# Kernel tuning notes

Measured on AMD Instinct MI355X. Metric: run time of the kernel, lower is better.

Reference implementation:

```python
import jax, jax.numpy as jnp
import numpy as np

IN_F, OUT_F, GROUP = 4096, 4096, 128
N_GROUPS = IN_F // GROUP  # 32


def setup_inputs() -> dict:
    key = jax.random.key(0)
    k1, k2, k3, k4, k5 = jax.random.split(key, 5)
    x = jax.random.normal(k1, (2, 1024, IN_F), dtype=jnp.float32)
    w_q = jax.random.randint(k2, (OUT_F, N_GROUPS, GROUP), -128, 128, dtype=jnp.int32)  # int8-range quantized weights
    s_w = jax.random.uniform(k3, (N_GROUPS, OUT_F), dtype=jnp.float32) * 0.01  # per-group, per-out-channel scales
    perm = jax.random.permutation(k4, IN_F).astype(jnp.int64)  # GPTQ activation-order permutation
    bias = jax.random.normal(k5, (OUT_F,), dtype=jnp.float32)
    return {"x": x, "w_q": w_q, "s_w": s_w, "perm": perm, "bias": bias}


def reference(x, w_q, s_w, perm, bias):
    prefix = x.shape[:-1]
    orig_dtype = x.dtype
    xf = x.reshape(-1, IN_F)          # (n, in)
    xf = xf[:, perm]                  # apply GPTQ permutation
    xf = xf.reshape(-1, N_GROUPS, GROUP).astype(jnp.float32)  # (n, g, k)
    wf = w_q.astype(jnp.float32)      # (o, g, k) dequant-to-fp32 weights (pre-scale)
    y_g = jnp.einsum('ngk,ogk->ngo', xf, wf)   # per-group partial products (n, g, o)
    y = jnp.sum(y_g * s_w[None, :, :], axis=1) # apply group scales, reduce groups -> (n, o)
    y = y + bias.astype(y.dtype)
    return y.reshape(*prefix, OUT_F).astype(orig_dtype)
```

## Files before the change

### kernel.cpp

```cpp
#include <hip/hip_runtime.h>
#include <hip/hip_bf16.h>
#include <stdint.h>

#define IN_F   4096
#define OUT_F  4096
#define M_ROWS 2048
#define NG     32
#define GRP    128

typedef __bf16 bf16x8 __attribute__((ext_vector_type(8)));
typedef float  f32x4  __attribute__((ext_vector_type(4)));

typedef const void __attribute__((address_space(1))) cv_g;
typedef void       __attribute__((address_space(3))) v_l;

__device__ __forceinline__ void async16(const void* g, void* l) {
  __builtin_amdgcn_global_load_lds((cv_g*)g, (v_l*)l, 16, 0, 0);
}

__device__ int g_perm_is64;

__global__ void decode_flag(const void* __restrict__ perm_raw) {
  if (threadIdx.x == 0 && blockIdx.x == 0) {
    const int* w = (const int*)perm_raw;
    int ok = 1;
    for (int j = 0; j < 32; ++j) {
      int lo = w[2 * j], hi = w[2 * j + 1];
      if (hi != 0 || lo < 0 || lo >= IN_F) { ok = 0; break; }
    }
    g_perm_is64 = ok;
  }
}

__global__ __launch_bounds__(256) void prep(const float* __restrict__ x,
                                            const int* __restrict__ w_q,
                                            const float* __restrict__ s_w,
                                            const void* __restrict__ perm_raw,
                                            __hip_bfloat16* __restrict__ xp,
                                            __hip_bfloat16* __restrict__ wf) {
  __shared__ float sx[IN_F];
  __shared__ int sflag;
  const int b = blockIdx.x;
  const int t = threadIdx.x;

  if (b < M_ROWS) {
    const int m = b;
    const float* xr = x + (size_t)m * IN_F;
#pragma unroll
    for (int u = 0; u < 4; ++u) {
      int idx = (u * 256 + t) * 4;
      *(float4*)&sx[idx] = *(const float4*)&xr[idx];
    }
    if (t < 64) {
      const int* w = (const int*)perm_raw;
      int j = t & 31;
      int lo = w[2 * j], hi = w[2 * j + 1];
      int cond = (hi == 0 && lo >= 0 && lo < IN_F);
      unsigned long long bal = __ballot(cond);
      if (t == 0) sflag = (bal == ~0ull) ? 1 : 0;
    }
    __syncthreads();
    const int f = sflag;
    const long long* p64 = (const long long*)perm_raw;
    const int*       p32 = (const int*)perm_raw;
    const int jb = t * 16;
    __hip_bfloat16 tmp[16] __attribute__((aligned(16)));
#pragma unroll
    for (int u = 0; u < 16; ++u) {
      int pj = f ? (int)p64[jb + u] : p32[jb + u];
      tmp[u] = __float2bfloat16(sx[pj]);
    }
    *(uint4*)(xp + (size_t)m * IN_F + jb)     = *(const uint4*)&tmp[0];
    *(uint4*)(xp + (size_t)m * IN_F + jb + 8) = *(const uint4*)&tmp[8];
  } else {
    int tt = (b - M_ROWS) * 256 + t;
    int o  = tt >> 9;
    int kb = (tt & 511) << 3;
    float s = s_w[(size_t)(kb >> 7) * OUT_F + o];
    const int* wr = w_q + (size_t)o * IN_F + kb;
    int4 w0 = *(const int4*)wr;
    int4 w1 = *(const int4*)(wr + 4);
    __hip_bfloat16 tmp[8] __attribute__((aligned(16)));
    tmp[0] = __float2bfloat16((float)w0.x * s);
    tmp[1] = __float2bfloat16((float)w0.y * s);
    tmp[2] = __float2bfloat16((float)w0.z * s);
    tmp[3] = __float2bfloat16((float)w0.w * s);
    tmp[4] = __float2bfloat16((float)w1.x * s);
    tmp[5] = __float2bfloat16((float)w1.y * s);
    tmp[6] = __float2bfloat16((float)w1.z * s);
    tmp[7] = __float2bfloat16((float)w1.w * s);
    *(uint4*)(wf + (size_t)o * IN_F + kb) = *(const uint4*)tmp;
  }
}

__global__ __launch_bounds__(256) void gemm_bt(
    const __hip_bfloat16* __restrict__ A,
    const __hip_bfloat16* __restrict__ B,
    const float* __restrict__ bias,
    float* __restrict__ C) {
  __shared__ __hip_bfloat16 sA[128 * 64];
  __shared__ __hip_bfloat16 sB[128 * 64];

  const int tid  = threadIdx.x;
  const int wave = tid >> 6;
  const int lane = tid & 63;
  const int bm = blockIdx.y << 7;
  const int bn = blockIdx.x << 7;
  const int wm = (wave >> 1) << 6;
  const int wn = (wave & 1) << 6;
  const int lrow = lane & 15;
  const int quad = lane >> 4;

  f32x4 acc[4][4] = {};

  const __hip_bfloat16* gA[4];
  const __hip_bfloat16* gB[4];
  __hip_bfloat16* lA[4];
  __hip_bfloat16* lB[4];
#pragma unroll
  for (int h = 0; h < 4; ++h) {
    int L   = h * 256 + wave * 64 + lane;
    int row = L >> 3;
    int kc  = (L & 7) ^ (row & 7);
    gA[h] = A + (size_t)(bm + row) * IN_F + kc * 8;
    gB[h] = B + (size_t)(bn + row) * IN_F + kc * 8;
    lA[h] = &sA[(h * 256 + wave * 64) * 8];
    lB[h] = &sB[(h * 256 + wave * 64) * 8];
  }

  for (int k0 = 0; k0 < IN_F; k0 += 64) {
#pragma unroll
    for (int h = 0; h < 4; ++h) {
      async16(gA[h] + k0, lA[h]);
      async16(gB[h] + k0, lB[h]);
    }
    __syncthreads();

#pragma unroll
    for (int s = 0; s < 2; ++s) {
      const int kcp = ((s << 2) + quad) ^ (lrow & 7);
      bf16x8 af[4], bfr[4];
#pragma unroll
      for (int i = 0; i < 4; ++i)
        af[i] = *(const bf16x8*)&sA[(wm + i * 16 + lrow) * 64 + kcp * 8];
#pragma unroll
      for (int j = 0; j < 4; ++j)
        bfr[j] = *(const bf16x8*)&sB[(wn + j * 16 + lrow) * 64 + kcp * 8];
#pragma unroll
      for (int i = 0; i < 4; ++i)
#pragma unroll
        for (int j = 0; j < 4; ++j)
          acc[i][j] = __builtin_amdgcn_mfma_f32_16x16x32_bf16(af[i], bfr[j], acc[i][j], 0, 0, 0);
    }

    __syncthreads();
  }

#pragma unroll
  for (int i = 0; i < 4; ++i) {
    int row = bm + wm + i * 16 + quad * 4;
#pragma unroll
    for (int j = 0; j < 4; ++j) {
      int col = bn + wn + j * 16 + lrow;
      float bv = bias[col];
#pragma unroll
      for (int r = 0; r < 4; ++r)
        C[(size_t)(row + r) * OUT_F + col] = acc[i][j][r] + bv;
    }
  }
}

__global__ void naive_fallback(const float* __restrict__ x, const int* __restrict__ w_q,
                               const float* __restrict__ s_w, const void* __restrict__ perm_raw,
                               const float* __restrict__ bias, float* __restrict__ out) {
  int t = blockIdx.x * blockDim.x + threadIdx.x;
  int m = t >> 12;
  int o = t & 4095;
  const int f = g_perm_is64;
  const long long* p64 = (const long long*)perm_raw;
  const int*       p32 = (const int*)perm_raw;
  const float* xr = x + (size_t)m * IN_F;
  const int*   wr = w_q + (size_t)o * IN_F;
  float acc = 0.f;
  for (int g = 0; g < NG; ++g) {
    float part = 0.f;
    for (int k = 0; k < GRP; ++k) {
      int j = g * GRP + k;
      int pj = f ? (int)p64[j] : p32[j];
      part += xr[pj] * (float)wr[j];
    }
    acc += part * s_w[(size_t)g * OUT_F + o];
  }
  out[t] = acc + bias[o];
}

extern "C" void kernel_launch(void* const* d_in, const int* in_sizes, int n_in,
                              void* d_out, int out_size, void* d_ws, size_t ws_size,
                              hipStream_t stream) {
  const float* x    = (const float*)d_in[0];
  const int*   w_q  = (const int*)d_in[1];
  const float* s_w  = (const float*)d_in[2];
  const void*  perm = d_in[3];
  const float* bias = (const float*)d_in[4];
  float* out = (float*)d_out;

  const size_t xp_bytes = (size_t)M_ROWS * IN_F * sizeof(__hip_bfloat16);
  const size_t wf_bytes = (size_t)OUT_F * IN_F * sizeof(__hip_bfloat16);

  if (ws_size < xp_bytes + wf_bytes) {
    decode_flag<<<1, 64, 0, stream>>>(perm);
    naive_fallback<<<(M_ROWS * OUT_F) / 256, 256, 0, stream>>>(x, w_q, s_w, perm, bias, out);
    return;
  }

  __hip_bfloat16* xp = (__hip_bfloat16*)d_ws;
  __hip_bfloat16* wf = (__hip_bfloat16*)((char*)d_ws + xp_bytes);

  prep<<<M_ROWS + (OUT_F * IN_F / 8) / 256, 256, 0, stream>>>(x, w_q, s_w, perm, xp, wf);

  dim3 grid(OUT_F / 128, M_ROWS / 128);
  gemm_bt<<<grid, 256, 0, stream>>>(xp, wf, bias, out);
}
```

Before: 219.7 us.

## Switch GEMM to int8 MFMA with per-row activation quantization and group-scale epilogue

The prep kernel now quantizes each permuted activation row to int8 using a per-row absmax scale, and narrows the int32 weights to raw int8 instead of dequantizing them to bf16. The GEMM runs int8 16x16x64 MFMAs into an int32 accumulator for each 128-wide group, then folds in that group's bf16-stored weight scale and the row scale in fp32. Loads are double-buffered in LDS with 256-wide K stages. The aim is to double MFMA throughput and halve operand traffic, at the cost of extra accuracy loss from int8 activations and per-group epilogue FMAs.

Result: faster. 195.4 us (-11.1%).

```diff
diff --git a/kernel.cpp b/kernel.cpp
--- a/kernel.cpp
+++ b/kernel.cpp
@@ -8,8 +8,8 @@
 #define NG     32
 #define GRP    128
 
-typedef __bf16 bf16x8 __attribute__((ext_vector_type(8)));
-typedef float  f32x4  __attribute__((ext_vector_type(4)));
+typedef int   v4i  __attribute__((ext_vector_type(4)));
+typedef float f32x4 __attribute__((ext_vector_type(4)));
 
 typedef const void __attribute__((address_space(1))) cv_g;
 typedef void       __attribute__((address_space(3))) v_l;
@@ -34,11 +34,12 @@
 
 __global__ __launch_bounds__(256) void prep(const float* __restrict__ x,
                                             const int* __restrict__ w_q,
-                                            const float* __restrict__ s_w,
                                             const void* __restrict__ perm_raw,
-                                            __hip_bfloat16* __restrict__ xp,
-                                            __hip_bfloat16* __restrict__ wf) {
+                                            char* __restrict__ xq,
+                                            char* __restrict__ w8,
+                                            float* __restrict__ sxr) {
   __shared__ float sx[IN_F];
+  __shared__ float red[4];
   __shared__ int sflag;
   const int b = blockIdx.x;
   const int t = threadIdx.x;
@@ -64,42 +65,54 @@
     const long long* p64 = (const long long*)perm_raw;
     const int*       p32 = (const int*)perm_raw;
     const int jb = t * 16;
-    __hip_bfloat16 tmp[16] __attribute__((aligned(16)));
+    float vals[16];
+    float lmax = 0.f;
 #pragma unroll
     for (int u = 0; u < 16; ++u) {
       int pj = f ? (int)p64[jb + u] : p32[jb + u];
-      tmp[u] = __float2bfloat16(sx[pj]);
-    }
-    *(uint4*)(xp + (size_t)m * IN_F + jb)     = *(const uint4*)&tmp[0];
-    *(uint4*)(xp + (size_t)m * IN_F + jb + 8) = *(const uint4*)&tmp[8];
+      float v = sx[pj];
+      vals[u] = v;
+      lmax = fmaxf(lmax, fabsf(v));
+    }
+#pragma unroll
+    for (int d = 1; d < 64; d <<= 1)
+      lmax = fmaxf(lmax, __shfl_xor(lmax, d, 64));
+    if ((t & 63) == 0) red[t >> 6] = lmax;
+    __syncthreads();
+    float rmax = fmaxf(fmaxf(red[0], red[1]), fmaxf(red[2], red[3]));
+    float inv = (rmax > 0.f) ? 127.f / rmax : 0.f;
+    if (t == 0) sxr[m] = rmax / 127.f;
+    char q[16] __attribute__((aligned(16)));
+#pragma unroll
+    for (int u = 0; u < 16; ++u)
+      q[u] = (char)__float2int_rn(vals[u] * inv);
+    *(uint4*)(xq + (size_t)m * IN_F + jb) = *(const uint4*)q;
   } else {
-    int tt = (b - M_ROWS) * 256 + t;
-    int o  = tt >> 9;
-    int kb = (tt & 511) << 3;
-    float s = s_w[(size_t)(kb >> 7) * OUT_F + o];
+    const int o  = b - M_ROWS;
+    const int kb = t * 16;
     const int* wr = w_q + (size_t)o * IN_F + kb;
-    int4 w0 = *(const int4*)wr;
+    int4 w0 = *(const int4*)(wr + 0);
     int4 w1 = *(const int4*)(wr + 4);
-    __hip_bfloat16 tmp[8] __attribute__((aligned(16)));
-    tmp[0] = __float2bfloat16((float)w0.x * s);
-    tmp[1] = __float2bfloat16((float)w0.y * s);
-    tmp[2] = __float2bfloat16((float)w0.z * s);
-    tmp[3] = __float2bfloat16((float)w0.w * s);
-    tmp[4] = __float2bfloat16((float)w1.x * s);
-    tmp[5] = __float2bfloat16((float)w1.y * s);
-    tmp[6] = __float2bfloat16((float)w1.z * s);
-    tmp[7] = __float2bfloat16((float)w1.w * s);
-    *(uint4*)(wf + (size_t)o * IN_F + kb) = *(const uint4*)tmp;
-  }
-}
-
-__global__ __launch_bounds__(256) void gemm_bt(
-    const __hip_bfloat16* __restrict__ A,
-    const __hip_bfloat16* __restrict__ B,
+    int4 w2 = *(const int4*)(wr + 8);
+    int4 w3 = *(const int4*)(wr + 12);
+    char q[16] __attribute__((aligned(16)));
+    q[0]=(char)w0.x; q[1]=(char)w0.y; q[2]=(char)w0.z; q[3]=(char)w0.w;
+    q[4]=(char)w1.x; q[5]=(char)w1.y; q[6]=(char)w1.z; q[7]=(char)w1.w;
+    q[8]=(char)w2.x; q[9]=(char)w2.y; q[10]=(char)w2.z; q[11]=(char)w2.w;
+    q[12]=(char)w3.x; q[13]=(char)w3.y; q[14]=(char)w3.z; q[15]=(char)w3.w;
+    *(uint4*)(w8 + (size_t)o * IN_F + kb) = *(const uint4*)q;
+  }
+}
+
+__global__ __launch_bounds__(256, 2) void gemm_i8(
+    const char* __restrict__ A,
+    const char* __restrict__ B,
+    const float* __restrict__ s_w,
+    const float* __restrict__ sxr,
     const float* __restrict__ bias,
     float* __restrict__ C) {
-  __shared__ __hip_bfloat16 sA[128 * 64];
-  __shared__ __hip_bfloat16 sB[128 * 64];
+  __shared__ char smem[2][32768];
+  __shared__ unsigned short sws[NG * 128];
 
   const int tid  = threadIdx.x;
   const int wave = tid >> 6;
@@ -111,61 +124,103 @@
   const int lrow = lane & 15;
   const int quad = lane >> 4;
 
-  f32x4 acc[4][4] = {};
-
-  const __hip_bfloat16* gA[4];
-  const __hip_bfloat16* gB[4];
-  __hip_bfloat16* lA[4];
-  __hip_bfloat16* lB[4];
-#pragma unroll
-  for (int h = 0; h < 4; ++h) {
-    int L   = h * 256 + wave * 64 + lane;
-    int row = L >> 3;
-    int kc  = (L & 7) ^ (row & 7);
-    gA[h] = A + (size_t)(bm + row) * IN_F + kc * 8;
-    gB[h] = B + (size_t)(bn + row) * IN_F + kc * 8;
-    lA[h] = &sA[(h * 256 + wave * 64) * 8];
-    lB[h] = &sB[(h * 256 + wave * 64) * 8];
-  }
-
-  for (int k0 = 0; k0 < IN_F; k0 += 64) {
-#pragma unroll
-    for (int h = 0; h < 4; ++h) {
-      async16(gA[h] + k0, lA[h]);
-      async16(gB[h] + k0, lB[h]);
-    }
-    __syncthreads();
-
+#pragma unroll
+  for (int u = 0; u < 16; ++u) {
+    int idx = u * 256 + tid;
+    int g = idx >> 7, c = idx & 127;
+    __hip_bfloat16 h = __float2bfloat16(s_w[(size_t)g * OUT_F + bn + c]);
+    sws[idx] = *(unsigned short*)&h;
+  }
+
+  f32x4 accf[4][4] = {};
+
+  const char* gp[8];
+  int lofs[8];
+#pragma unroll
+  for (int h = 0; h < 8; ++h) {
+    int c0 = (h * 4 + wave) * 64;
+    int c  = c0 + lane;
+    if (c < 1024) {
+      int row = c >> 3;
+      int kc  = (c & 7) ^ (row & 7);
+      gp[h]   = A + (size_t)(bm + row) * IN_F + kc * 16;
+      lofs[h] = c0 * 16;
+    } else {
+      int cb  = c - 1024;
+      int row = cb >> 3;
+      int kc  = (cb & 7) ^ (row & 7);
+      gp[h]   = B + (size_t)(bn + row) * IN_F + kc * 16;
+      lofs[h] = 16384 + (c0 - 1024) * 16;
+    }
+  }
+
+  auto stage = [&](int p, int kn) {
+#pragma unroll
+    for (int h = 0; h < 8; ++h)
+      async16(gp[h] + kn, &smem[p][lofs[h]]);
+  };
+
+  auto compute = [&](int p, int g) {
+    const char* bufA = smem[p];
+    const char* bufB = smem[p] + 16384;
+    v4i acci[4][4] = {};
 #pragma unroll
     for (int s = 0; s < 2; ++s) {
-      const int kcp = ((s << 2) + quad) ^ (lrow & 7);
-      bf16x8 af[4], bfr[4];
+      v4i af[4], bf[4];
+#pragma unroll
+      for (int i = 0; i < 4; ++i) {
+        int row = wm + i * 16 + lrow;
+        af[i] = *(const v4i*)&bufA[row * 128 + (((s << 2) + quad) ^ (row & 7)) * 16];
+      }
+#pragma unroll
+      for (int j = 0; j < 4; ++j) {
+        int row = wn + j * 16 + lrow;
+        bf[j] = *(const v4i*)&bufB[row * 128 + (((s << 2) + quad) ^ (row & 7)) * 16];
+      }
 #pragma unroll
       for (int i = 0; i < 4; ++i)
-        af[i] = *(const bf16x8*)&sA[(wm + i * 16 + lrow) * 64 + kcp * 8];
+#pragma unroll
+        for (int j = 0; j < 4; ++j)
+          acci[i][j] = __builtin_amdgcn_mfma_i32_16x16x64_i8(af[i], bf[j], acci[i][j], 0, 0, 0);
+    }
+    float swv[4];
+#pragma unroll
+    for (int j = 0; j < 4; ++j) {
+      unsigned int u = sws[g * 128 + wn + j * 16 + lrow];
+      swv[j] = __uint_as_float(u << 16);
+    }
+#pragma unroll
+    for (int i = 0; i < 4; ++i)
 #pragma unroll
       for (int j = 0; j < 4; ++j)
-        bfr[j] = *(const bf16x8*)&sB[(wn + j * 16 + lrow) * 64 + kcp * 8];
-#pragma unroll
-      for (int i = 0; i < 4; ++i)
-#pragma unroll
-        for (int j = 0; j < 4; ++j)
-          acc[i][j] = __builtin_amdgcn_mfma_f32_16x16x32_bf16(af[i], bfr[j], acc[i][j], 0, 0, 0);
-    }
-
-    __syncthreads();
+#pragma unroll
+        for (int r = 0; r < 4; ++r)
+          accf[i][j][r] += swv[j] * (float)acci[i][j][r];
+  };
+
+  stage(0, 0);
+  for (int k0 = 0; k0 < IN_F; k0 += 256) {
+    __syncthreads();
+    stage(1, k0 + 128);
+    compute(0, k0 >> 7);
+    __syncthreads();
+    if (k0 + 256 < IN_F) stage(0, k0 + 256);
+    compute(1, (k0 >> 7) + 1);
   }
 
 #pragma unroll
   for (int i = 0; i < 4; ++i) {
-    int row = bm + wm + i * 16 + quad * 4;
+    int r0 = bm + wm + i * 16 + quad * 4;
+    float sxv[4];
+#pragma unroll
+    for (int r = 0; r < 4; ++r) sxv[r] = sxr[r0 + r];
 #pragma unroll
     for (int j = 0; j < 4; ++j) {
       int col = bn + wn + j * 16 + lrow;
       float bv = bias[col];
 #pragma unroll
       for (int r = 0; r < 4; ++r)
-        C[(size_t)(row + r) * OUT_F + col] = acc[i][j][r] + bv;
+        C[(size_t)(r0 + r) * OUT_F + col] = sxv[r] * accf[i][j][r] + bv;
     }
   }
 }
@@ -204,20 +259,23 @@
   const float* bias = (const float*)d_in[4];
   float* out = (float*)d_out;
 
-  const size_t xp_bytes = (size_t)M_ROWS * IN_F * sizeof(__hip_bfloat16);
-  const size_t wf_bytes = (size_t)OUT_F * IN_F * sizeof(__hip_bfloat16);
-
-  if (ws_size < xp_bytes + wf_bytes) {
+  const size_t xq_bytes = (size_t)M_ROWS * IN_F;
+  const size_t w8_bytes = (size_t)OUT_F * IN_F;
+  const size_t sx_bytes = (size_t)M_ROWS * sizeof(float);
+  const size_t need = xq_bytes + w8_bytes + sx_bytes;
+
+  if (ws_size < need) {
     decode_flag<<<1, 64, 0, stream>>>(perm);
     naive_fallback<<<(M_ROWS * OUT_F) / 256, 256, 0, stream>>>(x, w_q, s_w, perm, bias, out);
     return;
   }
 
-  __hip_bfloat16* xp = (__hip_bfloat16*)d_ws;
-  __hip_bfloat16* wf = (__hip_bfloat16*)((char*)d_ws + xp_bytes);
-
-  prep<<<M_ROWS + (OUT_F * IN_F / 8) / 256, 256, 0, stream>>>(x, w_q, s_w, perm, xp, wf);
+  char*  xq  = (char*)d_ws;
+  char*  w8  = (char*)d_ws + xq_bytes;
+  float* sxr = (float*)((char*)d_ws + xq_bytes + w8_bytes);
+
+  prep<<<M_ROWS + OUT_F, 256, 0, stream>>>(x, w_q, perm, xq, w8, sxr);
 
   dim3 grid(OUT_F / 128, M_ROWS / 128);
-  gemm_bt<<<grid, 256, 0, stream>>>(xp, wf, bias, out);
-}
+  gemm_i8<<<grid, 256, 0, stream>>>(xq, w8, s_w, sxr, bias, out);
+}
```
